# Performance work log

Hardware: AMD Instinct MI355X
Metric: run time of the kernel (lower is better)

Reference implementation:

```python
import jax, jax.numpy as jnp
import numpy as np

T, D_MODEL, D_FF, N_EXPERTS, TOP_K = 8192, 1024, 4096, 8, 2

def setup_inputs() -> dict:
    key = jax.random.key(0)
    k1, k2, k3, k4, k5 = jax.random.split(key, 5)
    hidden_states = jax.random.normal(k1, (T, D_MODEL), dtype=jnp.float32)
    # router picks TOP_K distinct-ish experts per token; build one-hot mask [T, K, E]
    expert_idx = jax.random.randint(k2, (T, TOP_K), 0, N_EXPERTS)
    selected_experts = jax.nn.one_hot(expert_idx, N_EXPERTS, dtype=jnp.int32)
    rw = jax.random.uniform(k3, (T, TOP_K), dtype=jnp.float32)
    routing_weights = rw / jnp.sum(rw, axis=-1, keepdims=True)
    scale = 1.0 / np.sqrt(D_MODEL)
    wi = jax.random.normal(k4, (N_EXPERTS, D_FF, D_MODEL), dtype=jnp.float32) * scale
    wo = jax.random.normal(k5, (N_EXPERTS, D_MODEL, D_FF), dtype=jnp.float32) * (1.0 / np.sqrt(D_FF))
    return {"hidden_states": hidden_states, "selected_experts": selected_experts,
            "routing_weights": routing_weights, "wi": wi, "wo": wo}

def reference(hidden_states, selected_experts, routing_weights, wi, wo):
    # expert_mask: [E, K, T] (as in torch permute(2,1,0))
    mask = jnp.transpose(selected_experts, (2, 1, 0)).astype(hidden_states.dtype)
    # combined per-token weight for each expert: w[t, e] = sum_k mask[e,k,t]*routing_weights[t,k]
    w = jnp.einsum('ekt,tk->te', mask, routing_weights)
    out = jnp.zeros_like(hidden_states)
    # fixed small loop over experts; tokens not routed to expert e get weight 0,
    # so this is mathematically identical to the gather->MLP->scale->scatter-add.
    for e in range(wi.shape[0]):
        h = jax.nn.relu(hidden_states @ wi[e].T)     # [T, d_ff] (dropout is identity at eval)
        y = h @ wo[e].T                              # [T, d_model]
        out = out + w[:, e:e + 1] * y
    return out
```

## Files before the change

### kernel.cpp

```cpp
#include <hip/hip_runtime.h>
#include <hip/hip_bf16.h>


#define T_TOK   8192
#define D_MODEL 1024
#define D_FF    4096
#define NE      8
#define BM      128
#define BK      64
#define MT_MAX  136
#define ROWS_MAX (MT_MAX * 128)

typedef float f32x4 __attribute__((ext_vector_type(4)));
typedef short s16x8 __attribute__((ext_vector_type(8)));
typedef short s16x4 __attribute__((ext_vector_type(4)));
typedef unsigned short u16;

__device__ __forceinline__ u16 f2bf(float x) {
  __hip_bfloat16 h = __float2bfloat16(x);
  return *reinterpret_cast<u16*>(&h);
}

__device__ __forceinline__ s16x8 cvt8(float4 a, float4 b) {
  s16x8 v;
  v[0] = (short)f2bf(a.x); v[1] = (short)f2bf(a.y);
  v[2] = (short)f2bf(a.z); v[3] = (short)f2bf(a.w);
  v[4] = (short)f2bf(b.x); v[5] = (short)f2bf(b.y);
  v[6] = (short)f2bf(b.z); v[7] = (short)f2bf(b.w);
  return v;
}

__device__ __forceinline__ void gload_lds16(const void* g, void* l) {
  __builtin_amdgcn_global_load_lds((const __attribute__((address_space(1))) void*)g,
                                   (__attribute__((address_space(3))) void*)l,
                                   16, 0, 0);
}

__global__ void moe_route(const int* __restrict__ sel, const float* __restrict__ rw,
                          int* __restrict__ cnt, int* __restrict__ tidx,
                          float* __restrict__ tw) {
  int t = blockIdx.x * blockDim.x + threadIdx.x;
  if (t >= T_TOK) return;
  int e0 = 0, e1 = 0;
  #pragma unroll
  for (int e = 0; e < NE; ++e) {
    if (sel[t * 16 + e])     e0 = e;
    if (sel[t * 16 + 8 + e]) e1 = e;
  }
  float w0 = rw[2 * t], w1 = rw[2 * t + 1];
  if (e0 == e1) {
    int p = atomicAdd(&cnt[e0], 1);
    tidx[e0 * T_TOK + p] = t; tw[e0 * T_TOK + p] = w0 + w1;
  } else {
    int p = atomicAdd(&cnt[e0], 1);
    tidx[e0 * T_TOK + p] = t; tw[e0 * T_TOK + p] = w0;
    int q = atomicAdd(&cnt[e1], 1);
    tidx[e1 * T_TOK + q] = t; tw[e1 * T_TOK + q] = w1;
  }
}

__global__ void moe_tilemap(const int* __restrict__ cnt, const int* __restrict__ tidx,
                            const float* __restrict__ tw, int* __restrict__ tile_e,
                            int* __restrict__ tokr, float* __restrict__ wr) {
  int off[NE + 1];
  {
    int o = 0;
    #pragma unroll
    for (int e = 0; e < NE; ++e) { off[e] = o; o += (cnt[e] + 127) & ~127; }
    off[NE] = o;
  }
  const int total = off[NE];
  const int gid = blockIdx.x * blockDim.x + threadIdx.x;
  const int stride = gridDim.x * blockDim.x;
  for (int t = gid; t < MT_MAX; t += stride) {
    int r0 = t * 128; int e = -1;
    if (r0 < total) {
      #pragma unroll
      for (int i = NE - 1; i >= 0; --i) if (r0 >= off[i]) { e = i; break; }
    }
    tile_e[t] = e;
  }
  for (int i = gid; i < ROWS_MAX; i += stride) {
    if (i >= total) { tokr[i] = -1; wr[i] = 0.f; continue; }
    int e = 0;
    #pragma unroll
    for (int k = NE - 1; k >= 0; --k) if (i >= off[k]) { e = k; break; }
    int j = i - off[e];
    int ok = j < cnt[e];
    tokr[i] = ok ? tidx[e * T_TOK + j] : -1;
    wr[i]   = ok ? tw[e * T_TOK + j] : 0.f;
  }
}

__global__ void moe_gather_x(const float* __restrict__ hs, const int* __restrict__ tokr,
                             u16* __restrict__ Xg) {
  int row = blockIdx.x;
  int tok = tokr[row];
  int c = threadIdx.x * 4;
  u16* dst = Xg + (size_t)row * D_MODEL + c;
  s16x4 o;
  if (tok < 0) {
    o[0] = o[1] = o[2] = o[3] = 0;
  } else {
    float4 v = *(const float4*)(hs + (size_t)tok * D_MODEL + c);
    o[0] = (short)f2bf(v.x); o[1] = (short)f2bf(v.y);
    o[2] = (short)f2bf(v.z); o[3] = (short)f2bf(v.w);
  }
  *(s16x4*)dst = o;
}

__global__ void moe_cvt_w(const float* __restrict__ wi, const float* __restrict__ wo,
                          u16* __restrict__ wib, u16* __restrict__ wob) {
  const size_t NW = (size_t)NE * D_FF * D_MODEL;
  size_t i = ((size_t)blockIdx.x * blockDim.x + threadIdx.x) * 8;
  const float* src; u16* dst;
  if (i < NW) { src = wi + i; dst = wib + i; }
  else        { src = wo + (i - NW); dst = wob + (i - NW); }
  float4 a = *(const float4*)(src);
  float4 b = *(const float4*)(src + 4);
  *(s16x8*)dst = cvt8(a, b);
}

__global__ void moe_cvt_wi_s(const float* __restrict__ wi, u16* __restrict__ wis,
                             int W, int f0) {
  size_t i = ((size_t)blockIdx.x * blockDim.x + threadIdx.x) * 8;
  size_t per = (size_t)W * D_MODEL;
  int e = (int)(i / per); size_t r = i % per;
  const float* src = wi + ((size_t)e * D_FF + f0) * D_MODEL + r;
  float4 a = *(const float4*)src;
  float4 b = *(const float4*)(src + 4);
  *(s16x8*)(wis + i) = cvt8(a, b);
}

__global__ void moe_cvt_wo_s(const float* __restrict__ wo, u16* __restrict__ wos,
                             int W, int f0) {
  size_t i = ((size_t)blockIdx.x * blockDim.x + threadIdx.x) * 8;
  size_t per = (size_t)D_MODEL * W;
  int e = (int)(i / per); size_t r = i % per;
  int row = (int)(r / W), col = (int)(r % W);
  const float* src = wo + ((size_t)e * D_MODEL + row) * D_FF + f0 + col;
  float4 a = *(const float4*)src;
  float4 b = *(const float4*)(src + 4);
  *(s16x8*)(wos + i) = cvt8(a, b);
}

template <bool FULL>
__global__ __launch_bounds__(256, 4)
void moe_g1(const u16* __restrict__ Xg, const u16* __restrict__ wiP,
            const int* __restrict__ tile_e, u16* __restrict__ H,
            int W, int f0, int ntasks) {
  __shared__ u16 As[BM * BK];
  __shared__ u16 Bs[BM * BK];

  const int tid = threadIdx.x;
  const int lane = tid & 63, wv = tid >> 6;
  const int lg = lane >> 4, ll = lane & 15;
  const int wm = wv >> 1, wn = wv & 1;

  const int GR = gridDim.x;
  const int sbid = (blockIdx.x & 7) * (GR >> 3) + (blockIdx.x >> 3);

  for (int task = sbid; task < ntasks; task += GR) {
    const int mt = task % MT_MAX;
    const int nc = task / MT_MAX;
    const int e = tile_e[mt];
    if (e < 0) continue;
    const int grow0 = mt * 128;
    const int fl = nc * 128;

    const u16* abase0 = Xg + (size_t)grow0 * D_MODEL;
    const u16* bbase0 = wiP + (FULL ? ((size_t)e * D_FF + f0 + fl)
                                    : ((size_t)e * W + fl)) * D_MODEL;

    f32x4 acc[4][4];
    #pragma unroll
    for (int m = 0; m < 4; ++m)
      #pragma unroll
      for (int n = 0; n < 4; ++n) acc[m][n] = (f32x4){0.f, 0.f, 0.f, 0.f};

    for (int kk = 0; kk < D_MODEL / BK; ++kk) {
      __syncthreads();
      const u16* ab = abase0 + kk * BK;
      #pragma unroll
      for (int i = 0; i < 4; ++i) {
        int off = wv * 4096 + i * 1024 + lane * 16;
        int row = off >> 7, colb = off & 127;
        gload_lds16(ab + (size_t)row * D_MODEL + (colb >> 1), (char*)As + off);
      }
      const u16* bb = bbase0 + kk * BK;
      #pragma unroll
      for (int i = 0; i < 4; ++i) {
        int off = wv * 4096 + i * 1024 + lane * 16;
        int row = off >> 7, colb = off & 127;
        gload_lds16(bb + (size_t)row * D_MODEL + (colb >> 1), (char*)Bs + off);
      }
      __syncthreads();
      #pragma unroll
      for (int kb = 0; kb < 2; ++kb) {
        s16x8 af[4], bf[4];
        #pragma unroll
        for (int m = 0; m < 4; ++m)
          af[m] = *(const s16x8*)(As + (wm * 64 + m * 16 + ll) * BK + kb * 32 + lg * 8);
        #pragma unroll
        for (int n = 0; n < 4; ++n)
          bf[n] = *(const s16x8*)(Bs + (wn * 64 + n * 16 + ll) * BK + kb * 32 + lg * 8);
        #pragma unroll
        for (int m = 0; m < 4; ++m)
          #pragma unroll
          for (int n = 0; n < 4; ++n)
            acc[m][n] = __builtin_amdgcn_mfma_f32_16x16x32_bf16(af[m], bf[n], acc[m][n], 0, 0, 0);
      }
    }

    const int hc = fl + wn * 64 + ll;
    #pragma unroll
    for (int m = 0; m < 4; ++m) {
      #pragma unroll
      for (int r = 0; r < 4; ++r) {
        int row = grow0 + wm * 64 + m * 16 + lg * 4 + r;
        u16* hp = H + (size_t)row * W + hc;
        #pragma unroll
        for (int n = 0; n < 4; ++n) {
          float v = acc[m][n][r];
          hp[n * 16] = f2bf(v > 0.f ? v : 0.f);
        }
      }
    }
  }
}

template <bool FULL>
__global__ __launch_bounds__(256, 3)
void moe_g2(const u16* __restrict__ H, const u16* __restrict__ woP,
            const int* __restrict__ tile_e, const int* __restrict__ tokr,
            const float* __restrict__ wr, float* __restrict__ out,
            int W, int f0, int ntasks, int KCH) {
  __shared__ u16 As[BM * BK];
  __shared__ u16 Bs[BM * BK];
  __shared__ int s_tok[BM];
  __shared__ float s_w[BM];

  const int tid = threadIdx.x;
  const int lane = tid & 63, wv = tid >> 6;
  const int lg = lane >> 4, ll = lane & 15;
  const int wm = wv >> 1, wn = wv & 1;

  const int GR = gridDim.x;
  const int sbid = (blockIdx.x & 7) * (GR >> 3) + (blockIdx.x >> 3);

  for (int task = sbid; task < ntasks; task += GR) {
    const int mt = task % MT_MAX;
    const int rest = task / MT_MAX;
    const int dc = rest & 7;
    const int kc = rest >> 3;
    const int e = tile_e[mt];
    if (e < 0) continue;
    const int grow0 = mt * 128;
    const int dcol0 = dc * 128;

    __syncthreads();
    if (tid < BM) { s_tok[tid] = tokr[grow0 + tid]; s_w[tid] = wr[grow0 + tid]; }

    const u16* abase0 = H + (size_t)grow0 * W + (size_t)kc * KCH;
    const size_t bpitch = FULL ? (size_t)D_FF : (size_t)W;
    const u16* bbase0 = woP + ((size_t)e * D_MODEL + dcol0) * bpitch
                        + (FULL ? f0 : 0) + (size_t)kc * KCH;

    f32x4 acc[4][4];
    #pragma unroll
    for (int m = 0; m < 4; ++m)
      #pragma unroll
      for (int n = 0; n < 4; ++n) acc[m][n] = (f32x4){0.f, 0.f, 0.f, 0.f};

    for (int kk = 0; kk < KCH / BK; ++kk) {
      __syncthreads();
      const u16* ab = abase0 + kk * BK;
      #pragma unroll
      for (int i = 0; i < 4; ++i) {
        int off = wv * 4096 + i * 1024 + lane * 16;
        int row = off >> 7, colb = off & 127;
        gload_lds16(ab + (size_t)row * W + (colb >> 1), (char*)As + off);
      }
      const u16* bb = bbase0 + kk * BK;
      #pragma unroll
      for (int i = 0; i < 4; ++i) {
        int off = wv * 4096 + i * 1024 + lane * 16;
        int row = off >> 7, colb = off & 127;
        gload_lds16(bb + (size_t)row * bpitch + (colb >> 1), (char*)Bs + off);
      }
      __syncthreads();
      #pragma unroll
      for (int kb = 0; kb < 2; ++kb) {
        s16x8 af[4], bf[4];
        #pragma unroll
        for (int m = 0; m < 4; ++m)
          af[m] = *(const s16x8*)(As + (wm * 64 + m * 16 + ll) * BK + kb * 32 + lg * 8);
        #pragma unroll
        for (int n = 0; n < 4; ++n)
          bf[n] = *(const s16x8*)(Bs + (wn * 64 + n * 16 + ll) * BK + kb * 32 + lg * 8);
        #pragma unroll
        for (int m = 0; m < 4; ++m)
          #pragma unroll
          for (int n = 0; n < 4; ++n)
            acc[m][n] = __builtin_amdgcn_mfma_f32_16x16x32_bf16(af[m], bf[n], acc[m][n], 0, 0, 0);
      }
    }

    #pragma unroll
    for (int m = 0; m < 4; ++m) {
      #pragma unroll
      for (int r = 0; r < 4; ++r) {
        int row = wm * 64 + m * 16 + lg * 4 + r;
        int tok = s_tok[row];
        if (tok >= 0) {
          float w = s_w[row];
          float* op = out + (size_t)tok * D_MODEL + dcol0 + wn * 64 + ll;
          #pragma unroll
          for (int n = 0; n < 4; ++n)
            atomicAdd(op + n * 16, acc[m][n][r] * w);
        }
      }
    }
  }
}

extern "C" void kernel_launch(void* const* d_in, const int* in_sizes, int n_in,
                              void* d_out, int out_size, void* d_ws, size_t ws_size,
                              hipStream_t stream) {
  const float* hs  = (const float*)d_in[0];
  const int*   sel = (const int*)d_in[1];
  const float* rw  = (const float*)d_in[2];
  const float* wi  = (const float*)d_in[3];
  const float* wo  = (const float*)d_in[4];
  float* out = (float*)d_out;

  const size_t NW   = (size_t)NE * D_FF * D_MODEL;
  const size_t CTRL = 1u << 20;
  const size_t WB   = 2 * NW * sizeof(u16);
  const size_t XGB  = (size_t)ROWS_MAX * D_MODEL * 2;

  bool FULLW = true; int W = D_FF;
  {
    bool found = false;
    for (int f : {1, 2, 4, 8, 16}) {
      int Wc = D_FF / f;
      size_t need = CTRL + WB + XGB + (size_t)ROWS_MAX * Wc * 2;
      if (need <= ws_size) { FULLW = true; W = Wc; found = true; break; }
    }
    if (!found) {
      for (int Wc : {1024, 512, 256}) {
        size_t sl = (size_t)2 * NE * Wc * D_MODEL * 2;
        size_t need = CTRL + sl + XGB + (size_t)ROWS_MAX * Wc * 2;
        if (need <= ws_size) { FULLW = false; W = Wc; break; }
      }
    }
  }
  const int FS = D_FF / W;

  size_t off = 0;
  auto take = [&](size_t b) -> char* {
    char* r = (char*)d_ws + off; off = (off + b + 255) & ~(size_t)255; return r;
  };
  int*   tidx = (int*)take((size_t)NE * T_TOK * 4);
  float* tw   = (float*)take((size_t)NE * T_TOK * 4);
  int*   tokr = (int*)take((size_t)ROWS_MAX * 4);
  float* wrr  = (float*)take((size_t)ROWS_MAX * 4);
  int*   te   = (int*)take(MT_MAX * 4);
  int*   cnt  = (int*)take(256);
  off = CTRL;
  u16 *wiP, *woP;
  if (FULLW) { wiP = (u16*)take(NW * 2); woP = (u16*)take(NW * 2); }
  else       { wiP = (u16*)take((size_t)NE * W * D_MODEL * 2);
               woP = (u16*)take((size_t)NE * D_MODEL * W * 2); }
  u16* Xg   = (u16*)take(XGB);
  u16* Hbuf = (u16*)take((size_t)ROWS_MAX * W * 2);

  hipMemsetAsync(cnt, 0, 256, stream);
  hipMemsetAsync(d_out, 0, (size_t)out_size * sizeof(float), stream);
  moe_route<<<T_TOK / 256, 256, 0, stream>>>(sel, rw, cnt, tidx, tw);
  moe_tilemap<<<64, 256, 0, stream>>>(cnt, tidx, tw, te, tokr, wrr);
  moe_gather_x<<<ROWS_MAX, 256, 0, stream>>>(hs, tokr, Xg);
  if (FULLW)
    moe_cvt_w<<<(int)(2 * NW / 8 / 256), 256, 0, stream>>>(wi, wo, wiP, woP);

  const int KCH = (W >= 2048) ? 2048 : W;
  const int nt1 = MT_MAX * (W / 128);
  const int nt2 = MT_MAX * 8 * (W / KCH);
  const int cvtblk = (int)(((size_t)NE * W * D_MODEL / 8) / 256);

  for (int p = 0; p < FS; ++p) {
    const int f0 = p * W;
    if (!FULLW) {
      moe_cvt_wi_s<<<cvtblk, 256, 0, stream>>>(wi, wiP, W, f0);
      moe_cvt_wo_s<<<cvtblk, 256, 0, stream>>>(wo, woP, W, f0);
    }
    if (FULLW) {
      moe_g1<true><<<1024, 256, 0, stream>>>(Xg, wiP, te, Hbuf, W, f0, nt1);
      moe_g2<true><<<768, 256, 0, stream>>>(Hbuf, woP, te, tokr, wrr, out, W, f0, nt2, KCH);
    } else {
      moe_g1<false><<<1024, 256, 0, stream>>>(Xg, wiP, te, Hbuf, W, f0, nt1);
      moe_g2<false><<<768, 256, 0, stream>>>(Hbuf, woP, te, tokr, wrr, out, W, f0, nt2, KCH);
    }
  }
}
```

Before: 624.3 us.

## Launch one block per GEMM tile instead of persistent grid-stride loops

Both expert GEMM kernels drop their persistent grid-stride task loops. Each launches a grid sized to the task count, so every block handles exactly one tile and returns early when the tile is unused. The block-index swizzle is kept. In the down-projection kernel the task decode now puts the output-column chunk in the fastest-varying position, so neighbouring blocks share the same H row tile, and its occupancy hint rises from 3 to 4 blocks per CU. This targets tail imbalance and register pressure from the loop. The trade-off is more block launches, plus some that exit immediately on empty tiles.

```diff
diff --git a/kernel.cpp b/kernel.cpp
--- a/kernel.cpp
+++ b/kernel.cpp
@@ -148,177 +148,171 @@
 __global__ __launch_bounds__(256, 4)
 void moe_g1(const u16* __restrict__ Xg, const u16* __restrict__ wiP,
             const int* __restrict__ tile_e, u16* __restrict__ H,
-            int W, int f0, int ntasks) {
+            int W, int f0) {
   __shared__ u16 As[BM * BK];
   __shared__ u16 Bs[BM * BK];
+
+  const int GR = gridDim.x;
+  const int task = (blockIdx.x & 7) * (GR >> 3) + (blockIdx.x >> 3);
+  const int mt = task % MT_MAX;
+  const int nc = task / MT_MAX;
+  const int e = tile_e[mt];
+  if (e < 0) return;
+  const int grow0 = mt * 128;
+  const int fl = nc * 128;
 
   const int tid = threadIdx.x;
   const int lane = tid & 63, wv = tid >> 6;
   const int lg = lane >> 4, ll = lane & 15;
   const int wm = wv >> 1, wn = wv & 1;
 
-  const int GR = gridDim.x;
-  const int sbid = (blockIdx.x & 7) * (GR >> 3) + (blockIdx.x >> 3);
-
-  for (int task = sbid; task < ntasks; task += GR) {
-    const int mt = task % MT_MAX;
-    const int nc = task / MT_MAX;
-    const int e = tile_e[mt];
-    if (e < 0) continue;
-    const int grow0 = mt * 128;
-    const int fl = nc * 128;
-
-    const u16* abase0 = Xg + (size_t)grow0 * D_MODEL;
-    const u16* bbase0 = wiP + (FULL ? ((size_t)e * D_FF + f0 + fl)
-                                    : ((size_t)e * W + fl)) * D_MODEL;
-
-    f32x4 acc[4][4];
-    #pragma unroll
-    for (int m = 0; m < 4; ++m)
-      #pragma unroll
-      for (int n = 0; n < 4; ++n) acc[m][n] = (f32x4){0.f, 0.f, 0.f, 0.f};
-
-    for (int kk = 0; kk < D_MODEL / BK; ++kk) {
-      __syncthreads();
-      const u16* ab = abase0 + kk * BK;
-      #pragma unroll
-      for (int i = 0; i < 4; ++i) {
-        int off = wv * 4096 + i * 1024 + lane * 16;
-        int row = off >> 7, colb = off & 127;
-        gload_lds16(ab + (size_t)row * D_MODEL + (colb >> 1), (char*)As + off);
-      }
-      const u16* bb = bbase0 + kk * BK;
-      #pragma unroll
-      for (int i = 0; i < 4; ++i) {
-        int off = wv * 4096 + i * 1024 + lane * 16;
-        int row = off >> 7, colb = off & 127;
-        gload_lds16(bb + (size_t)row * D_MODEL + (colb >> 1), (char*)Bs + off);
-      }
-      __syncthreads();
-      #pragma unroll
-      for (int kb = 0; kb < 2; ++kb) {
-        s16x8 af[4], bf[4];
-        #pragma unroll
-        for (int m = 0; m < 4; ++m)
-          af[m] = *(const s16x8*)(As + (wm * 64 + m * 16 + ll) * BK + kb * 32 + lg * 8);
+  const u16* abase0 = Xg + (size_t)grow0 * D_MODEL;
+  const u16* bbase0 = wiP + (FULL ? ((size_t)e * D_FF + f0 + fl)
+                                  : ((size_t)e * W + fl)) * D_MODEL;
+
+  f32x4 acc[4][4];
+  #pragma unroll
+  for (int m = 0; m < 4; ++m)
+    #pragma unroll
+    for (int n = 0; n < 4; ++n) acc[m][n] = (f32x4){0.f, 0.f, 0.f, 0.f};
+
+  for (int kk = 0; kk < D_MODEL / BK; ++kk) {
+    __syncthreads();
+    const u16* ab = abase0 + kk * BK;
+    #pragma unroll
+    for (int i = 0; i < 4; ++i) {
+      int off = wv * 4096 + i * 1024 + lane * 16;
+      int row = off >> 7, colb = off & 127;
+      gload_lds16(ab + (size_t)row * D_MODEL + (colb >> 1), (char*)As + off);
+    }
+    const u16* bb = bbase0 + kk * BK;
+    #pragma unroll
+    for (int i = 0; i < 4; ++i) {
+      int off = wv * 4096 + i * 1024 + lane * 16;
+      int row = off >> 7, colb = off & 127;
+      gload_lds16(bb + (size_t)row * D_MODEL + (colb >> 1), (char*)Bs + off);
+    }
+    __syncthreads();
+    #pragma unroll
+    for (int kb = 0; kb < 2; ++kb) {
+      s16x8 af[4], bf[4];
+      #pragma unroll
+      for (int m = 0; m < 4; ++m)
+        af[m] = *(const s16x8*)(As + (wm * 64 + m * 16 + ll) * BK + kb * 32 + lg * 8);
+      #pragma unroll
+      for (int n = 0; n < 4; ++n)
+        bf[n] = *(const s16x8*)(Bs + (wn * 64 + n * 16 + ll) * BK + kb * 32 + lg * 8);
+      #pragma unroll
+      for (int m = 0; m < 4; ++m)
         #pragma unroll
         for (int n = 0; n < 4; ++n)
-          bf[n] = *(const s16x8*)(Bs + (wn * 64 + n * 16 + ll) * BK + kb * 32 + lg * 8);
-        #pragma unroll
-        for (int m = 0; m < 4; ++m)
-          #pragma unroll
-          for (int n = 0; n < 4; ++n)
-            acc[m][n] = __builtin_amdgcn_mfma_f32_16x16x32_bf16(af[m], bf[n], acc[m][n], 0, 0, 0);
+          acc[m][n] = __builtin_amdgcn_mfma_f32_16x16x32_bf16(af[m], bf[n], acc[m][n], 0, 0, 0);
+    }
+  }
+
+  const int hc = fl + wn * 64 + ll;
+  #pragma unroll
+  for (int m = 0; m < 4; ++m) {
+    #pragma unroll
+    for (int r = 0; r < 4; ++r) {
+      int row = grow0 + wm * 64 + m * 16 + lg * 4 + r;
+      u16* hp = H + (size_t)row * W + hc;
+      #pragma unroll
+      for (int n = 0; n < 4; ++n) {
+        float v = acc[m][n][r];
+        hp[n * 16] = f2bf(v > 0.f ? v : 0.f);
       }
     }
-
-    const int hc = fl + wn * 64 + ll;
-    #pragma unroll
-    for (int m = 0; m < 4; ++m) {
-      #pragma unroll
-      for (int r = 0; r < 4; ++r) {
-        int row = grow0 + wm * 64 + m * 16 + lg * 4 + r;
-        u16* hp = H + (size_t)row * W + hc;
-        #pragma unroll
-        for (int n = 0; n < 4; ++n) {
-          float v = acc[m][n][r];
-          hp[n * 16] = f2bf(v > 0.f ? v : 0.f);
-        }
-      }
-    }
   }
 }
 
 template <bool FULL>
-__global__ __launch_bounds__(256, 3)
+__global__ __launch_bounds__(256, 4)
 void moe_g2(const u16* __restrict__ H, const u16* __restrict__ woP,
             const int* __restrict__ tile_e, const int* __restrict__ tokr,
             const float* __restrict__ wr, float* __restrict__ out,
-            int W, int f0, int ntasks, int KCH) {
+            int W, int f0, int KCH) {
   __shared__ u16 As[BM * BK];
   __shared__ u16 Bs[BM * BK];
   __shared__ int s_tok[BM];
   __shared__ float s_w[BM];
 
+  const int GR = gridDim.x;
+  const int task = (blockIdx.x & 7) * (GR >> 3) + (blockIdx.x >> 3);
+  const int dc = task & 7;
+  const int rest = task >> 3;
+  const int mt = rest % MT_MAX;
+  const int kc = rest / MT_MAX;
+  const int e = tile_e[mt];
+  if (e < 0) return;
+  const int grow0 = mt * 128;
+  const int dcol0 = dc * 128;
+
   const int tid = threadIdx.x;
   const int lane = tid & 63, wv = tid >> 6;
   const int lg = lane >> 4, ll = lane & 15;
   const int wm = wv >> 1, wn = wv & 1;
 
-  const int GR = gridDim.x;
-  const int sbid = (blockIdx.x & 7) * (GR >> 3) + (blockIdx.x >> 3);
-
-  for (int task = sbid; task < ntasks; task += GR) {
-    const int mt = task % MT_MAX;
-    const int rest = task / MT_MAX;
-    const int dc = rest & 7;
-    const int kc = rest >> 3;
-    const int e = tile_e[mt];
-    if (e < 0) continue;
-    const int grow0 = mt * 128;
-    const int dcol0 = dc * 128;
-
+  if (tid < BM) { s_tok[tid] = tokr[grow0 + tid]; s_w[tid] = wr[grow0 + tid]; }
+  __syncthreads();
+
+  const u16* abase0 = H + (size_t)grow0 * W + (size_t)kc * KCH;
+  const size_t bpitch = FULL ? (size_t)D_FF : (size_t)W;
+  const u16* bbase0 = woP + ((size_t)e * D_MODEL + dcol0) * bpitch
+                      + (FULL ? f0 : 0) + (size_t)kc * KCH;
+
+  f32x4 acc[4][4];
+  #pragma unroll
+  for (int m = 0; m < 4; ++m)
+    #pragma unroll
+    for (int n = 0; n < 4; ++n) acc[m][n] = (f32x4){0.f, 0.f, 0.f, 0.f};
+
+  for (int kk = 0; kk < KCH / BK; ++kk) {
     __syncthreads();
-    if (tid < BM) { s_tok[tid] = tokr[grow0 + tid]; s_w[tid] = wr[grow0 + tid]; }
-
-    const u16* abase0 = H + (size_t)grow0 * W + (size_t)kc * KCH;
-    const size_t bpitch = FULL ? (size_t)D_FF : (size_t)W;
-    const u16* bbase0 = woP + ((size_t)e * D_MODEL + dcol0) * bpitch
-                        + (FULL ? f0 : 0) + (size_t)kc * KCH;
-
-    f32x4 acc[4][4];
-    #pragma unroll
-    for (int m = 0; m < 4; ++m)
-      #pragma unroll
-      for (int n = 0; n < 4; ++n) acc[m][n] = (f32x4){0.f, 0.f, 0.f, 0.f};
-
-    for (int kk = 0; kk < KCH / BK; ++kk) {
-      __syncthreads();
-      const u16* ab = abase0 + kk * BK;
-      #pragma unroll
-      for (int i = 0; i < 4; ++i) {
-        int off = wv * 4096 + i * 1024 + lane * 16;
-        int row = off >> 7, colb = off & 127;
-        gload_lds16(ab + (size_t)row * W + (colb >> 1), (char*)As + off);
-      }
-      const u16* bb = bbase0 + kk * BK;
-      #pragma unroll
-      for (int i = 0; i < 4; ++i) {
-        int off = wv * 4096 + i * 1024 + lane * 16;
-        int row = off >> 7, colb = off & 127;
-        gload_lds16(bb + (size_t)row * bpitch + (colb >> 1), (char*)Bs + off);
-      }
-      __syncthreads();
-      #pragma unroll
-      for (int kb = 0; kb < 2; ++kb) {
-        s16x8 af[4], bf[4];
-        #pragma unroll
-        for (int m = 0; m < 4; ++m)
-          af[m] = *(const s16x8*)(As + (wm * 64 + m * 16 + ll) * BK + kb * 32 + lg * 8);
+    const u16* ab = abase0 + kk * BK;
+    #pragma unroll
+    for (int i = 0; i < 4; ++i) {
+      int off = wv * 4096 + i * 1024 + lane * 16;
+      int row = off >> 7, colb = off & 127;
+      gload_lds16(ab + (size_t)row * W + (colb >> 1), (char*)As + off);
+    }
+    const u16* bb = bbase0 + kk * BK;
+    #pragma unroll
+    for (int i = 0; i < 4; ++i) {
+      int off = wv * 4096 + i * 1024 + lane * 16;
+      int row = off >> 7, colb = off & 127;
+      gload_lds16(bb + (size_t)row * bpitch + (colb >> 1), (char*)Bs + off);
+    }
+    __syncthreads();
+    #pragma unroll
+    for (int kb = 0; kb < 2; ++kb) {
+      s16x8 af[4], bf[4];
+      #pragma unroll
+      for (int m = 0; m < 4; ++m)
+        af[m] = *(const s16x8*)(As + (wm * 64 + m * 16 + ll) * BK + kb * 32 + lg * 8);
+      #pragma unroll
+      for (int n = 0; n < 4; ++n)
+        bf[n] = *(const s16x8*)(Bs + (wn * 64 + n * 16 + ll) * BK + kb * 32 + lg * 8);
+      #pragma unroll
+      for (int m = 0; m < 4; ++m)
         #pragma unroll
         for (int n = 0; n < 4; ++n)
-          bf[n] = *(const s16x8*)(Bs + (wn * 64 + n * 16 + ll) * BK + kb * 32 + lg * 8);
+          acc[m][n] = __builtin_amdgcn_mfma_f32_16x16x32_bf16(af[m], bf[n], acc[m][n], 0, 0, 0);
+    }
+  }
+
+  #pragma unroll
+  for (int m = 0; m < 4; ++m) {
+    #pragma unroll
+    for (int r = 0; r < 4; ++r) {
+      int row = wm * 64 + m * 16 + lg * 4 + r;
+      int tok = s_tok[row];
+      if (tok >= 0) {
+        float w = s_w[row];
+        float* op = out + (size_t)tok * D_MODEL + dcol0 + wn * 64 + ll;
         #pragma unroll
-        for (int m = 0; m < 4; ++m)
-          #pragma unroll
-          for (int n = 0; n < 4; ++n)
-            acc[m][n] = __builtin_amdgcn_mfma_f32_16x16x32_bf16(af[m], bf[n], acc[m][n], 0, 0, 0);
-      }
-    }
-
-    #pragma unroll
-    for (int m = 0; m < 4; ++m) {
-      #pragma unroll
-      for (int r = 0; r < 4; ++r) {
-        int row = wm * 64 + m * 16 + lg * 4 + r;
-        int tok = s_tok[row];
-        if (tok >= 0) {
-          float w = s_w[row];
-          float* op = out + (size_t)tok * D_MODEL + dcol0 + wn * 64 + ll;
-          #pragma unroll
-          for (int n = 0; n < 4; ++n)
-            atomicAdd(op + n * 16, acc[m][n][r] * w);
-        }
+        for (int n = 0; n < 4; ++n)
+          atomicAdd(op + n * 16, acc[m][n][r] * w);
       }
     }
   }
@@ -384,8 +378,8 @@
     moe_cvt_w<<<(int)(2 * NW / 8 / 256), 256, 0, stream>>>(wi, wo, wiP, woP);
 
   const int KCH = (W >= 2048) ? 2048 : W;
-  const int nt1 = MT_MAX * (W / 128);
-  const int nt2 = MT_MAX * 8 * (W / KCH);
+  const int g1grid = MT_MAX * (W / 128);
+  const int g2grid = MT_MAX * 8 * (W / KCH);
   const int cvtblk = (int)(((size_t)NE * W * D_MODEL / 8) / 256);
 
   for (int p = 0; p < FS; ++p) {
@@ -395,11 +389,11 @@
       moe_cvt_wo_s<<<cvtblk, 256, 0, stream>>>(wo, woP, W, f0);
     }
     if (FULLW) {
-      moe_g1<true><<<1024, 256, 0, stream>>>(Xg, wiP, te, Hbuf, W, f0, nt1);
-      moe_g2<true><<<768, 256, 0, stream>>>(Hbuf, woP, te, tokr, wrr, out, W, f0, nt2, KCH);
+      moe_g1<true><<<g1grid, 256, 0, stream>>>(Xg, wiP, te, Hbuf, W, f0);
+      moe_g2<true><<<g2grid, 256, 0, stream>>>(Hbuf, woP, te, tokr, wrr, out, W, f0, KCH);
     } else {
-      moe_g1<false><<<1024, 256, 0, stream>>>(Xg, wiP, te, Hbuf, W, f0, nt1);
-      moe_g2<false><<<768, 256, 0, stream>>>(Hbuf, woP, te, tokr, wrr, out, W, f0, nt2, KCH);
-    }
-  }
-}
+      moe_g1<false><<<g1grid, 256, 0, stream>>>(Xg, wiP, te, Hbuf, W, f0);
+      moe_g2<false><<<g2grid, 256, 0, stream>>>(Hbuf, woP, te, tokr, wrr, out, W, f0, KCH);
+    }
+  }
+}
```

New measurement: 571.7 us. 1.09x faster.
